# Optimization experiments

Hardware: AMD Instinct MI355X
Metric: run time of the kernel (lower is better)

The kernel has to match this reference:

```python
import jax, jax.numpy as jnp
import numpy as np
import math

B, S, D, H = 4, 2048, 1024, 16
DH = D // H  # 64
DFF = 4 * D
EPS = 1e-5


def layer_norm(x, g, b):
    mu = jnp.mean(x, axis=-1, keepdims=True)
    var = jnp.mean(jnp.square(x - mu), axis=-1, keepdims=True)
    return (x - mu) * jax.lax.rsqrt(var + EPS) * g + b


def apply_rope(xq, xk, freqs_cis):
    # xq, xk: [B, S, H, DH]; freqs_cis: [S, DH//2, 2] (cos, sin)
    cos = freqs_cis[None, :, None, :, 0]  # [1, S, 1, DH//2]
    sin = freqs_cis[None, :, None, :, 1]

    def rot(t):
        tr = t.reshape(*t.shape[:-1], DH // 2, 2)
        t0, t1 = tr[..., 0], tr[..., 1]
        o0 = t0 * cos - t1 * sin
        o1 = t0 * sin + t1 * cos
        return jnp.stack([o0, o1], axis=-1).reshape(t.shape)

    return rot(xq), rot(xk)


def setup_inputs() -> dict:
    key = jax.random.key(0)
    ks = jax.random.split(key, 12)
    x = jax.random.normal(ks[0], (B, S, D), dtype=jnp.float32)
    # rotary frequencies (theta = 10000), stored as (cos, sin)
    inv = 1.0 / (10000.0 ** (np.arange(0, DH, 2, dtype=np.float32) / DH))
    t = np.arange(S, dtype=np.float32)
    ang = np.outer(t, inv)  # [S, DH//2]
    freqs_cis = jnp.asarray(np.stack([np.cos(ang), np.sin(ang)], axis=-1))
    s = 1.0 / math.sqrt(D)
    sf = 1.0 / math.sqrt(DFF)
    return {
        "x": x,
        "freqs_cis": freqs_cis,
        "wq": jax.random.normal(ks[1], (D, D), dtype=jnp.float32) * s,
        "wk": jax.random.normal(ks[2], (D, D), dtype=jnp.float32) * s,
        "wv": jax.random.normal(ks[3], (D, D), dtype=jnp.float32) * s,
        "w_proj": jax.random.normal(ks[4], (D, D), dtype=jnp.float32) * s,
        "b_proj": jnp.zeros((D,), dtype=jnp.float32),
        "w_ff1": jax.random.normal(ks[5], (D, DFF), dtype=jnp.float32) * s,
        "b_ff1": jnp.zeros((DFF,), dtype=jnp.float32),
        "w_ff2": jax.random.normal(ks[6], (DFF, D), dtype=jnp.float32) * sf,
        "b_ff2": jnp.zeros((D,), dtype=jnp.float32),
        "ln1_g": jnp.ones((D,), dtype=jnp.float32),
        "ln1_b": jnp.zeros((D,), dtype=jnp.float32),
        "ln2_g": jnp.ones((D,), dtype=jnp.float32),
        "ln2_b": jnp.zeros((D,), dtype=jnp.float32),
    }


def reference(x, freqs_cis, wq, wk, wv, w_proj, b_proj, w_ff1, b_ff1, w_ff2,
              b_ff2, ln1_g, ln1_b, ln2_g, ln2_b):
    # --- attention block (pre-norm) ---
    h = layer_norm(x, ln1_g, ln1_b)
    xq = (h @ wq).reshape(B, S, H, DH)
    xk = (h @ wk).reshape(B, S, H, DH)
    xv = (h @ wv).reshape(B, S, H, DH)
    xq, xk = apply_rope(xq, xk, freqs_cis)
    # [B, H, S, S]
    att = jnp.einsum("bqhd,bkhd->bhqk", xq, xk) / math.sqrt(DH)
    att = jax.nn.softmax(att, axis=-1)
    out = jnp.einsum("bhqk,bkhd->bqhd", att, xv).reshape(B, S, D)
    x = x + out @ w_proj + b_proj
    # --- feed-forward block (pre-norm, GELU) ---
    h2 = layer_norm(x, ln2_g, ln2_b)
    ff = jax.nn.gelu(h2 @ w_ff1 + b_ff1, approximate=False) @ w_ff2 + b_ff2
    return x + ff
```

## Files before the change

### kernel.cpp

```cpp
#include <hip/hip_runtime.h>
#include <hip/hip_bf16.h>


#define Bb_ 4
#define Ss_ 2048
#define Dd_ 1024
#define Hh_ 16
#define DFF_ 4096

typedef __bf16 bf16x8 __attribute__((ext_vector_type(8)));
typedef float f32x4 __attribute__((ext_vector_type(4)));

static __device__ __forceinline__ unsigned short f2bf(float f) {
  union { float f; unsigned u; } v; v.f = f;
  unsigned r = v.u + 0x7FFF + ((v.u >> 16) & 1);
  return (unsigned short)(r >> 16);
}
static __device__ __forceinline__ float bf2f(unsigned short h) {
  union { unsigned u; float f; } v; v.u = ((unsigned)h) << 16;
  return v.f;
}
static __device__ __forceinline__ unsigned cvt_pk_bf16(float lo, float hi) {
  unsigned r;
  asm("v_cvt_pk_bf16_f32 %0, %1, %2" : "=v"(r) : "v"(lo), "v"(hi));
  return r;
}

static __device__ __forceinline__ void gl16(const unsigned short* g, void* l) {
  __builtin_amdgcn_global_load_lds(
      (const __attribute__((address_space(1))) void*)g,
      (__attribute__((address_space(3))) void*)l, 16, 0, 0);
}

__global__ __launch_bounds__(256) void ln_kernel(
    const float* __restrict__ x, const float* __restrict__ g,
    const float* __restrict__ bb, unsigned short* __restrict__ out)
{
  const int row = blockIdx.x;
  const int t = threadIdx.x;
  const float4 v = reinterpret_cast<const float4*>(x + (size_t)row * Dd_)[t];
  float s = v.x + v.y + v.z + v.w;
  float ss = v.x*v.x + v.y*v.y + v.z*v.z + v.w*v.w;
  #pragma unroll
  for (int o = 32; o; o >>= 1) { s += __shfl_down(s, o); ss += __shfl_down(ss, o); }
  __shared__ float red[8];
  if ((t & 63) == 0) { red[t >> 6] = s; red[4 + (t >> 6)] = ss; }
  __syncthreads();
  s = red[0] + red[1] + red[2] + red[3];
  ss = red[4] + red[5] + red[6] + red[7];
  const float mean = s * (1.f / Dd_);
  const float var = ss * (1.f / Dd_) - mean * mean;
  const float inv = rsqrtf(var + 1e-5f);
  const float4 gv = reinterpret_cast<const float4*>(g)[t];
  const float4 bv = reinterpret_cast<const float4*>(bb)[t];
  ushort4 o4;
  o4.x = f2bf((v.x - mean) * inv * gv.x + bv.x);
  o4.y = f2bf((v.y - mean) * inv * gv.y + bv.y);
  o4.z = f2bf((v.z - mean) * inv * gv.z + bv.z);
  o4.w = f2bf((v.w - mean) * inv * gv.w + bv.w);
  reinterpret_cast<ushort4*>(out + (size_t)row * Dd_)[t] = o4;
}

__global__ __launch_bounds__(256) void tconv_kernel(
    const float* __restrict__ src, unsigned short* __restrict__ dst, int K, int N)
{
  __shared__ float tile[32][33];
  const int bx = blockIdx.x, by = blockIdx.y;
  const int tx = threadIdx.x & 31, ty = threadIdx.x >> 5;
  #pragma unroll
  for (int i = 0; i < 4; i++)
    tile[ty + i * 8][tx] = src[(size_t)(by * 32 + ty + i * 8) * N + bx * 32 + tx];
  __syncthreads();
  #pragma unroll
  for (int i = 0; i < 4; i++)
    dst[(size_t)(bx * 32 + ty + i * 8) * K + by * 32 + tx] = f2bf(tile[tx][ty + i * 8]);
}

__global__ __launch_bounds__(256) void rope_kernel(
    unsigned short* __restrict__ qkv, const float* __restrict__ fc)
{
  const int c = blockIdx.x * 256 + threadIdx.x;
  const int row = c >> 8;
  const int rem = c & 255;
  const int qk = rem >> 7;
  const int e8 = rem & 127;
  const int s = row & (Ss_ - 1);
  const float4 f0 = *reinterpret_cast<const float4*>(fc + s * 64 + (e8 & 7) * 8);
  const float4 f1 = *reinterpret_cast<const float4*>(fc + s * 64 + (e8 & 7) * 8 + 4);
  unsigned short* p = qkv + (size_t)row * 3072 + qk * 1024 + e8 * 8;
  uint4 dv = *reinterpret_cast<const uint4*>(p);
  unsigned u[4] = {dv.x, dv.y, dv.z, dv.w};
  const float cs[8] = {f0.x, f0.y, f0.z, f0.w, f1.x, f1.y, f1.z, f1.w};
  #pragma unroll
  for (int j = 0; j < 4; j++) {
    const float t0 = bf2f((unsigned short)(u[j] & 0xffff));
    const float t1 = bf2f((unsigned short)(u[j] >> 16));
    const float cj = cs[2 * j], sj = cs[2 * j + 1];
    const float o0 = t0 * cj - t1 * sj;
    const float o1 = t0 * sj + t1 * cj;
    u[j] = (unsigned)f2bf(o0) | ((unsigned)f2bf(o1) << 16);
  }
  uint4 ov; ov.x = u[0]; ov.y = u[1]; ov.z = u[2]; ov.w = u[3];
  *reinterpret_cast<uint4*>(p) = ov;
}

__global__ __launch_bounds__(256) void vtrans_kernel(
    const unsigned short* __restrict__ qkv, unsigned short* __restrict__ vt)
{
  __shared__ unsigned short tile[64 * 64];
  const int st = blockIdx.x, h = blockIdx.y, b = blockIdx.z;
  const int t = threadIdx.x;
  const unsigned short* src = qkv + (size_t)(b * Ss_ + st * 64) * 3072 + 2048 + h * 64;
  {
    const int s = t >> 2;
    const int v = (s >> 3) & 7;
    #pragma unroll
    for (int j = 0; j < 2; j++) {
      const int col8 = (t & 3) * 2 + j;
      const uint4 d = *reinterpret_cast<const uint4*>(src + (size_t)s * 3072 + col8 * 8);
      *reinterpret_cast<uint4*>(&tile[s * 64 + ((col8 * 8) ^ (v * 8))]) = d;
    }
  }
  __syncthreads();
  unsigned short* dst = vt + (size_t)((b * 16 + h) * 64) * Ss_ + st * 64;
  #pragma unroll
  for (int it = 0; it < 2; it++) {
    const int c = t + it * 256;
    const int d = c >> 3, s8 = c & 7;
    unsigned short o[8];
    #pragma unroll
    for (int j = 0; j < 8; j++) {
      const int s = s8 * 8 + j;
      o[j] = tile[s * 64 + (d ^ (((s >> 3) & 7) * 8))];
    }
    *reinterpret_cast<uint4*>(dst + (size_t)d * Ss_ + s8 * 8) = *reinterpret_cast<uint4*>(o);
  }
}

template<int MODE>
__global__ __launch_bounds__(256) void gemm_kernel(
    const unsigned short* __restrict__ A,
    const unsigned short* __restrict__ BT,
    int K, int nbn, int N,
    const float* __restrict__ bias,
    const float* __restrict__ resid,
    void* __restrict__ out)
{
  __shared__ unsigned short As[2][128 * 64];
  __shared__ unsigned short Bs[2][128 * 64];
  const int t = threadIdx.x;

  const int nwg = gridDim.x;
  const int id = blockIdx.x;
  const int sid = (id & 7) * (nwg >> 3) + (id >> 3);
  const int bm = sid / nbn, bn = sid % nbn;

  const int w = t >> 6, lane = t & 63;
  const int lq = lane >> 4, lr = lane & 15;
  const int wm = (w >> 1) * 64, wn = (w & 1) * 64;
  const int srow = t >> 3, sg8 = t & 7;
  const int sw8 = sg8 ^ (srow & 7);

  const unsigned short* ag = A  + (size_t)(bm * 128 + srow) * K + sw8 * 8;
  const unsigned short* bg = BT + (size_t)(bn * 128 + srow) * K + sw8 * 8;

  char* AsB = (char*)As;
  char* BsB = (char*)Bs;
  const int csw = (lr & 7) * 8;
  int aoffB[2], boffB[2];
  aoffB[0] = (wm + lr) * 128 + 2 * ((lq * 8) ^ csw);
  aoffB[1] = (wm + lr) * 128 + 2 * ((32 + lq * 8) ^ csw);
  boffB[0] = (wn + lr) * 128 + 2 * ((lq * 8) ^ csw);
  boffB[1] = (wn + lr) * 128 + 2 * ((32 + lq * 8) ^ csw);
  const int sdstB = (srow * 64 + sg8 * 8) * 2;

  f32x4 acc[4][4] = {};
  const int nt = K >> 6;

#define STAGE7(BUF)                                                          \
  {                                                                          \
    _Pragma("unroll")                                                        \
    for (int i_ = 0; i_ < 4; i_++) {                                         \
      gl16(ag + (size_t)i_ * 32 * K, AsB + (BUF) * 16384 + sdstB + i_ * 4096); \
      gl16(bg + (size_t)i_ * 32 * K, BsB + (BUF) * 16384 + sdstB + i_ * 4096); \
    }                                                                        \
    ag += 64; bg += 64;                                                      \
  }

#define COMPUTE7(BUF)                                                        \
  {                                                                          \
    __builtin_amdgcn_s_setprio(1);                                           \
    _Pragma("unroll")                                                        \
    for (int kc_ = 0; kc_ < 2; kc_++) {                                      \
      bf16x8 af[4], bfr[4];                                                  \
      _Pragma("unroll")                                                      \
      for (int i_ = 0; i_ < 4; i_++) {                                       \
        af[i_]  = *reinterpret_cast<const bf16x8*>(AsB + (BUF) * 16384 + aoffB[kc_] + i_ * 2048); \
        bfr[i_] = *reinterpret_cast<const bf16x8*>(BsB + (BUF) * 16384 + boffB[kc_] + i_ * 2048); \
      }                                                                      \
      _Pragma("unroll")                                                      \
      for (int i_ = 0; i_ < 4; i_++)                                         \
        _Pragma("unroll")                                                    \
        for (int j_ = 0; j_ < 4; j_++)                                       \
          acc[i_][j_] = __builtin_amdgcn_mfma_f32_16x16x32_bf16(af[i_], bfr[j_], acc[i_][j_], 0, 0, 0); \
    }                                                                        \
    __builtin_amdgcn_s_setprio(0);                                           \
  }

  STAGE7(0);
  __syncthreads();
  for (int t0 = 0; t0 < nt; t0 += 2) {
    STAGE7(1);
    COMPUTE7(0);
    __syncthreads();
    if (t0 + 2 < nt) STAGE7(0);
    COMPUTE7(1);
    __syncthreads();
  }
#undef STAGE7
#undef COMPUTE7

  const int growbase = bm * 128 + wm + lq * 4;
  const int gcolbase = bn * 128 + wn + lr;
  #pragma unroll
  for (int j = 0; j < 4; j++) {
    const int col = gcolbase + j * 16;
    const float bj = (MODE != 0) ? bias[col] : 0.f;
    #pragma unroll
    for (int i = 0; i < 4; i++) {
      #pragma unroll
      for (int r = 0; r < 4; r++) {
        const int grow = growbase + i * 16 + r;
        const float v = acc[i][j][r];
        if (MODE == 0) {
          ((unsigned short*)out)[(size_t)grow * N + col] = f2bf(v);
        } else if (MODE == 1 || MODE == 3) {
          ((float*)out)[(size_t)grow * N + col] = v + bj + resid[(size_t)grow * N + col];
        } else {
          const float u = v + bj;
          const float gel = 0.5f * u * (1.f + erff(u * 0.70710678118654752f));
          ((unsigned short*)out)[(size_t)grow * N + col] = f2bf(gel);
        }
      }
    }
  }
}

__global__ __launch_bounds__(256) void attn_kernel(
    const unsigned short* __restrict__ qkv,
    const unsigned short* __restrict__ vt,
    unsigned short* __restrict__ attout)
{
  __shared__ unsigned short Ks[2][64 * 64];
  __shared__ unsigned short Vs[2][64 * 64];
  __shared__ unsigned short Ps[128 * 64];
  const int qt = blockIdx.x, h = blockIdx.y, b = blockIdx.z;
  const int t = threadIdx.x, w = t >> 6, lane = t & 63;
  const int lq = lane >> 4, lr = lane & 15;
  const int srow = t >> 3, sg8 = t & 7;

  const unsigned short* kg = qkv + (size_t)(b * Ss_) * 3072 + 1024 + h * 64;
  const unsigned short* vg = vt + (size_t)((b * 16 + h) * 64) * Ss_;

  bf16x8 aq[2][2];
  {
    const unsigned short* qg = qkv + (size_t)(b * Ss_ + qt * 128) * 3072 + h * 64;
    #pragma unroll
    for (int mt = 0; mt < 2; mt++)
      #pragma unroll
      for (int kc = 0; kc < 2; kc++)
        aq[mt][kc] = *reinterpret_cast<const bf16x8*>(
            qg + (size_t)(w * 32 + mt * 16 + lr) * 3072 + kc * 32 + lq * 8);
  }

  bf16x8 ones;
  #pragma unroll
  for (int j = 0; j < 8; j++) ones[j] = (__bf16)1.0f;

  f32x4 oacc[2][4] = {};
  f32x4 ssum[2] = {};

  const int g8s0 = sg8 ^ ((srow)      & 7);
  const int g8s1 = sg8 ^ ((srow + 32) & 7);

  {
    gl16(kg + (size_t)(srow)      * 3072 + g8s0 * 8, &Ks[0][(srow)      * 64 + sg8 * 8]);
    gl16(kg + (size_t)(srow + 32) * 3072 + g8s1 * 8, &Ks[0][(srow + 32) * 64 + sg8 * 8]);
    gl16(vg + (size_t)(srow)      * Ss_  + g8s0 * 8, &Vs[0][(srow)      * 64 + sg8 * 8]);
    gl16(vg + (size_t)(srow + 32) * Ss_  + g8s1 * 8, &Vs[0][(srow + 32) * 64 + sg8 * 8]);
  }
  __syncthreads();

  const float SC2 = 0.125f * 1.44269504088896f;

  for (int kt = 0; kt < Ss_ / 64; ++kt) {
    const int cur = kt & 1;
    if (kt < Ss_ / 64 - 1) {
      const int nb = cur ^ 1;
      const size_t ko = (size_t)((kt + 1) * 64);
      gl16(kg + (ko + srow)      * 3072 + g8s0 * 8, &Ks[nb][(srow)      * 64 + sg8 * 8]);
      gl16(kg + (ko + srow + 32) * 3072 + g8s1 * 8, &Ks[nb][(srow + 32) * 64 + sg8 * 8]);
      gl16(vg + (size_t)(srow)      * Ss_ + (kt + 1) * 64 + g8s0 * 8, &Vs[nb][(srow)      * 64 + sg8 * 8]);
      gl16(vg + (size_t)(srow + 32) * Ss_ + (kt + 1) * 64 + g8s1 * 8, &Vs[nb][(srow + 32) * 64 + sg8 * 8]);
    }

    f32x4 sacc[2][4] = {};
    #pragma unroll
    for (int kc = 0; kc < 2; kc++) {
      const int cofs = kc * 32 + lq * 8;
      const int swz = (lr & 7) * 8;
      bf16x8 kb[4];
      #pragma unroll
      for (int nf = 0; nf < 4; nf++)
        kb[nf] = *reinterpret_cast<const bf16x8*>(&Ks[cur][(nf * 16 + lr) * 64 + (cofs ^ swz)]);
      #pragma unroll
      for (int mt = 0; mt < 2; mt++)
        #pragma unroll
        for (int nf = 0; nf < 4; nf++)
          sacc[mt][nf] = __builtin_amdgcn_mfma_f32_16x16x32_bf16(kb[nf], aq[mt][kc], sacc[mt][nf], 0, 0, 0);
    }

    #pragma unroll
    for (int mt = 0; mt < 2; mt++) {
      const int qrow = w * 32 + mt * 16 + lr;
      char* prow = reinterpret_cast<char*>(Ps) + qrow * 128;
      const int sw = (lr & 7) << 4;
      #pragma unroll
      for (int nf = 0; nf < 4; nf++) {
        const float p0 = __builtin_amdgcn_exp2f(sacc[mt][nf][0] * SC2);
        const float p1 = __builtin_amdgcn_exp2f(sacc[mt][nf][1] * SC2);
        const float p2 = __builtin_amdgcn_exp2f(sacc[mt][nf][2] * SC2);
        const float p3 = __builtin_amdgcn_exp2f(sacc[mt][nf][3] * SC2);
        uint2 pw;
        pw.x = cvt_pk_bf16(p0, p1);
        pw.y = cvt_pk_bf16(p2, p3);
        *reinterpret_cast<uint2*>(prow + ((nf * 32 + lq * 8) ^ sw)) = pw;
      }
    }

    #pragma unroll
    for (int kc = 0; kc < 2; kc++) {
      const int cofs = kc * 32 + lq * 8;
      const int swz = (lr & 7) * 8;
      bf16x8 pa[2], vb[4];
      #pragma unroll
      for (int mt = 0; mt < 2; mt++) {
        const int qrow = w * 32 + mt * 16 + lr;
        pa[mt] = *reinterpret_cast<const bf16x8*>(
            reinterpret_cast<const char*>(Ps) + qrow * 128 + ((kc * 64 + lq * 16) ^ ((lr & 7) << 4)));
      }
      #pragma unroll
      for (int mt = 0; mt < 2; mt++)
        ssum[mt] = __builtin_amdgcn_mfma_f32_16x16x32_bf16(pa[mt], ones, ssum[mt], 0, 0, 0);
      #pragma unroll
      for (int nf = 0; nf < 4; nf++)
        vb[nf] = *reinterpret_cast<const bf16x8*>(&Vs[cur][(nf * 16 + lr) * 64 + (cofs ^ swz)]);
      #pragma unroll
      for (int mt = 0; mt < 2; mt++)
        #pragma unroll
        for (int nf = 0; nf < 4; nf++)
          oacc[mt][nf] = __builtin_amdgcn_mfma_f32_16x16x32_bf16(pa[mt], vb[nf], oacc[mt][nf], 0, 0, 0);
    }

    __syncthreads();
  }

  #pragma unroll
  for (int mt = 0; mt < 2; mt++) {
    #pragma unroll
    for (int r = 0; r < 4; r++) {
      const float inv = 1.f / ssum[mt][r];
      const int grow = b * Ss_ + qt * 128 + w * 32 + mt * 16 + lq * 4 + r;
      #pragma unroll
      for (int nf = 0; nf < 4; nf++)
        attout[(size_t)grow * Dd_ + h * 64 + nf * 16 + lr] = f2bf(oacc[mt][nf][r] * inv);
    }
  }
}

extern "C" void kernel_launch(void* const* d_in, const int* in_sizes, int n_in,
                              void* d_out, int out_size, void* d_ws, size_t ws_size,
                              hipStream_t stream) {
  const float* x      = (const float*)d_in[0];
  const float* fc     = (const float*)d_in[1];
  const float* wq     = (const float*)d_in[2];
  const float* wk     = (const float*)d_in[3];
  const float* wv     = (const float*)d_in[4];
  const float* w_proj = (const float*)d_in[5];
  const float* b_proj = (const float*)d_in[6];
  const float* w_ff1  = (const float*)d_in[7];
  const float* b_ff1  = (const float*)d_in[8];
  const float* w_ff2  = (const float*)d_in[9];
  const float* b_ff2  = (const float*)d_in[10];
  const float* ln1_g  = (const float*)d_in[11];
  const float* ln1_b  = (const float*)d_in[12];
  const float* ln2_g  = (const float*)d_in[13];
  const float* ln2_b  = (const float*)d_in[14];

  char* ws = (char*)d_ws;
  unsigned short* hb     = (unsigned short*)(ws);
  unsigned short* wqkvT  = (unsigned short*)(ws + 16777216ull);
  unsigned short* wprojT = (unsigned short*)(ws + 23068672ull);
  unsigned short* wff1T  = (unsigned short*)(ws + 25165824ull);
  unsigned short* wff2T  = (unsigned short*)(ws + 33554432ull);
  float*          x2     = (float*)(ws + 41943040ull);
  unsigned short* vtb    = (unsigned short*)(ws + 41943040ull);
  unsigned short* attoutb= (unsigned short*)(ws + 75497472ull);
  unsigned short* qkvb   = (unsigned short*)(ws + 92274688ull);
  unsigned short* ff1b   = qkvb;

  dim3 blk(256);

  tconv_kernel<<<dim3(32, 32), blk, 0, stream>>>(wq, wqkvT, 1024, 1024);
  tconv_kernel<<<dim3(32, 32), blk, 0, stream>>>(wk, wqkvT + 1024 * 1024, 1024, 1024);
  tconv_kernel<<<dim3(32, 32), blk, 0, stream>>>(wv, wqkvT + 2 * 1024 * 1024, 1024, 1024);
  tconv_kernel<<<dim3(32, 32), blk, 0, stream>>>(w_proj, wprojT, 1024, 1024);
  tconv_kernel<<<dim3(128, 32), blk, 0, stream>>>(w_ff1, wff1T, 1024, 4096);
  tconv_kernel<<<dim3(32, 128), blk, 0, stream>>>(w_ff2, wff2T, 4096, 1024);

  ln_kernel<<<8192, blk, 0, stream>>>(x, ln1_g, ln1_b, hb);
  gemm_kernel<0><<<1536, blk, 0, stream>>>(hb, wqkvT, 1024, 24, 3072, nullptr, nullptr, qkvb);
  rope_kernel<<<8192, blk, 0, stream>>>(qkvb, fc);
  vtrans_kernel<<<dim3(32, 16, 4), blk, 0, stream>>>(qkvb, vtb);
  attn_kernel<<<dim3(16, 16, 4), blk, 0, stream>>>(qkvb, vtb, attoutb);
  gemm_kernel<1><<<512, blk, 0, stream>>>(attoutb, wprojT, 1024, 8, 1024, b_proj, x, x2);
  ln_kernel<<<8192, blk, 0, stream>>>(x2, ln2_g, ln2_b, hb);
  gemm_kernel<2><<<2048, blk, 0, stream>>>(hb, wff1T, 1024, 32, 4096, b_ff1, nullptr, ff1b);
  gemm_kernel<3><<<512, blk, 0, stream>>>(ff1b, wff2T, 4096, 8, 1024, b_ff2, x2, (float*)d_out);
}
```

Before: 428.3 us.

## Add 256x256-tile 8-wave GEMM for QKV and FF1 projections

Adds a new GEMM kernel with 256x256 output tiles, 512 threads and 64 KB LDS double buffering. It uses explicit barrier/waitcnt interleaving so the global-to-LDS loads of the next K tile overlap MFMA work, and raises MFMA priority with setprio. The QKV and FF1 GEMMs now use it, which halves operand traffic per flop compared with the 128x128 kernel. The cost is lower occupancy (one block per CU, high register use). With only 384 and 512 blocks the grid may not balance well across CUs.

```diff
diff --git a/kernel.cpp b/kernel.cpp
--- a/kernel.cpp
+++ b/kernel.cpp
@@ -134,6 +134,150 @@
       o[j] = tile[s * 64 + (d ^ (((s >> 3) & 7) * 8))];
     }
     *reinterpret_cast<uint4*>(dst + (size_t)d * Ss_ + s8 * 8) = *reinterpret_cast<uint4*>(o);
+  }
+}
+
+template<int MODE>
+__global__ __launch_bounds__(512, 1) void gemm256_kernel(
+    const unsigned short* __restrict__ A,
+    const unsigned short* __restrict__ BT,
+    int K, int nbn, int N,
+    const float* __restrict__ bias,
+    void* __restrict__ out)
+{
+  __shared__ __align__(16) unsigned short As[2][256 * 64];
+  __shared__ __align__(16) unsigned short Bs[2][256 * 64];
+  const int t = threadIdx.x;
+
+  const int nwg = gridDim.x;
+  const int id = blockIdx.x;
+  const int sid = (id & 7) * (nwg >> 3) + (id >> 3);
+  const int bm = sid / nbn, bn = sid % nbn;
+
+  const int w = t >> 6, lane = t & 63;
+  const int lq = lane >> 4, lr = lane & 15;
+  const int wr = w >> 2, wc = w & 3;
+  const int srow = t >> 3, sg8 = t & 7;
+  const int sw8 = sg8 ^ (srow & 7);
+
+  const unsigned short* ag = A  + (size_t)(bm * 256 + srow) * K + sw8 * 8;
+  const unsigned short* bg = BT + (size_t)(bn * 256 + srow) * K + sw8 * 8;
+
+  char* AsB = (char*)As;
+  char* BsB = (char*)Bs;
+  const int aRow = (wr * 128 + lr) * 128;
+  const int bRow = (wc * 64 + lr) * 128;
+  int cofs[2];
+  cofs[0] = 2 * ((lq * 8) ^ ((lr & 7) * 8));
+  cofs[1] = 2 * (((32 + lq * 8)) ^ ((lr & 7) * 8));
+  const int sdst = (srow * 64 + sg8 * 8) * 2;
+
+  f32x4 acc[8][4] = {};
+  bf16x8 a0, a1, a2, a3, b0, b1, b2, b3;
+  const int nt = K >> 6;
+
+#define BAR_   __builtin_amdgcn_s_barrier()
+#define LGKM0_ { asm volatile("s_waitcnt lgkmcnt(0)" ::: "memory"); __builtin_amdgcn_sched_barrier(0); }
+#define VM0_   { asm volatile("s_waitcnt vmcnt(0)" ::: "memory"); __builtin_amdgcn_sched_barrier(0); }
+
+#define RD_A(D, MH, KC)                                                       \
+  a0 = *reinterpret_cast<const bf16x8*>(AsB + (D) * 32768 + aRow + (MH) * 8192 + 0 * 2048 + cofs[KC]); \
+  a1 = *reinterpret_cast<const bf16x8*>(AsB + (D) * 32768 + aRow + (MH) * 8192 + 1 * 2048 + cofs[KC]); \
+  a2 = *reinterpret_cast<const bf16x8*>(AsB + (D) * 32768 + aRow + (MH) * 8192 + 2 * 2048 + cofs[KC]); \
+  a3 = *reinterpret_cast<const bf16x8*>(AsB + (D) * 32768 + aRow + (MH) * 8192 + 3 * 2048 + cofs[KC]);
+
+#define RD_B(D, KC)                                                           \
+  b0 = *reinterpret_cast<const bf16x8*>(BsB + (D) * 32768 + bRow + 0 * 2048 + cofs[KC]); \
+  b1 = *reinterpret_cast<const bf16x8*>(BsB + (D) * 32768 + bRow + 1 * 2048 + cofs[KC]); \
+  b2 = *reinterpret_cast<const bf16x8*>(BsB + (D) * 32768 + bRow + 2 * 2048 + cofs[KC]); \
+  b3 = *reinterpret_cast<const bf16x8*>(BsB + (D) * 32768 + bRow + 3 * 2048 + cofs[KC]);
+
+#define MM_(MH)                                                               \
+  {                                                                           \
+    __builtin_amdgcn_s_setprio(1);                                            \
+    acc[(MH)*4+0][0] = __builtin_amdgcn_mfma_f32_16x16x32_bf16(a0, b0, acc[(MH)*4+0][0], 0, 0, 0); \
+    acc[(MH)*4+0][1] = __builtin_amdgcn_mfma_f32_16x16x32_bf16(a0, b1, acc[(MH)*4+0][1], 0, 0, 0); \
+    acc[(MH)*4+0][2] = __builtin_amdgcn_mfma_f32_16x16x32_bf16(a0, b2, acc[(MH)*4+0][2], 0, 0, 0); \
+    acc[(MH)*4+0][3] = __builtin_amdgcn_mfma_f32_16x16x32_bf16(a0, b3, acc[(MH)*4+0][3], 0, 0, 0); \
+    acc[(MH)*4+1][0] = __builtin_amdgcn_mfma_f32_16x16x32_bf16(a1, b0, acc[(MH)*4+1][0], 0, 0, 0); \
+    acc[(MH)*4+1][1] = __builtin_amdgcn_mfma_f32_16x16x32_bf16(a1, b1, acc[(MH)*4+1][1], 0, 0, 0); \
+    acc[(MH)*4+1][2] = __builtin_amdgcn_mfma_f32_16x16x32_bf16(a1, b2, acc[(MH)*4+1][2], 0, 0, 0); \
+    acc[(MH)*4+1][3] = __builtin_amdgcn_mfma_f32_16x16x32_bf16(a1, b3, acc[(MH)*4+1][3], 0, 0, 0); \
+    acc[(MH)*4+2][0] = __builtin_amdgcn_mfma_f32_16x16x32_bf16(a2, b0, acc[(MH)*4+2][0], 0, 0, 0); \
+    acc[(MH)*4+2][1] = __builtin_amdgcn_mfma_f32_16x16x32_bf16(a2, b1, acc[(MH)*4+2][1], 0, 0, 0); \
+    acc[(MH)*4+2][2] = __builtin_amdgcn_mfma_f32_16x16x32_bf16(a2, b2, acc[(MH)*4+2][2], 0, 0, 0); \
+    acc[(MH)*4+2][3] = __builtin_amdgcn_mfma_f32_16x16x32_bf16(a2, b3, acc[(MH)*4+2][3], 0, 0, 0); \
+    acc[(MH)*4+3][0] = __builtin_amdgcn_mfma_f32_16x16x32_bf16(a3, b0, acc[(MH)*4+3][0], 0, 0, 0); \
+    acc[(MH)*4+3][1] = __builtin_amdgcn_mfma_f32_16x16x32_bf16(a3, b1, acc[(MH)*4+3][1], 0, 0, 0); \
+    acc[(MH)*4+3][2] = __builtin_amdgcn_mfma_f32_16x16x32_bf16(a3, b2, acc[(MH)*4+3][2], 0, 0, 0); \
+    acc[(MH)*4+3][3] = __builtin_amdgcn_mfma_f32_16x16x32_bf16(a3, b3, acc[(MH)*4+3][3], 0, 0, 0); \
+    __builtin_amdgcn_s_setprio(0);                                            \
+  }
+
+#define STG_A(D)                                                              \
+  gl16(ag,                   AsB + (D) * 32768 + sdst);                       \
+  gl16(ag + (size_t) 64 * K, AsB + (D) * 32768 + sdst + 8192);                \
+  gl16(ag + (size_t)128 * K, AsB + (D) * 32768 + sdst + 16384);               \
+  gl16(ag + (size_t)192 * K, AsB + (D) * 32768 + sdst + 24576);
+
+#define STG_B(D)                                                              \
+  gl16(bg,                   BsB + (D) * 32768 + sdst);                       \
+  gl16(bg + (size_t) 64 * K, BsB + (D) * 32768 + sdst + 8192);                \
+  gl16(bg + (size_t)128 * K, BsB + (D) * 32768 + sdst + 16384);               \
+  gl16(bg + (size_t)192 * K, BsB + (D) * 32768 + sdst + 24576);
+
+#define KSTEP(D, HN)                                                          \
+  {                                                                           \
+     RD_A(D, 0, 0); RD_B(D, 0); if (HN) { STG_A((D) ^ 1); }           \
+    BAR_; LGKM0_; MM_(0); BAR_;                                               \
+     RD_A(D, 1, 0);             if (HN) { STG_B((D) ^ 1); }           \
+    BAR_; LGKM0_; MM_(1); BAR_;                                               \
+     RD_A(D, 0, 1); RD_B(D, 1);                                       \
+    BAR_; LGKM0_; MM_(0); BAR_;                                               \
+     RD_A(D, 1, 1);                                                   \
+    BAR_; LGKM0_; MM_(1); VM0_; BAR_;                                         \
+    ag += 64; bg += 64;                                                       \
+  }
+
+  STG_A(0); STG_B(0);
+  ag += 64; bg += 64;
+  VM0_; BAR_;
+
+  for (int t0 = 0; t0 < nt - 2; t0 += 2) { KSTEP(0, 1); KSTEP(1, 1); }
+  KSTEP(0, 1);
+  KSTEP(1, 0);
+
+#undef KSTEP
+#undef STG_A
+#undef STG_B
+#undef MM_
+#undef RD_A
+#undef RD_B
+#undef BAR_
+#undef LGKM0_
+#undef VM0_
+
+  const int growbase = bm * 256 + wr * 128 + lq * 4;
+  const int gcolbase = bn * 256 + wc * 64 + lr;
+  #pragma unroll
+  for (int j = 0; j < 4; j++) {
+    const int col = gcolbase + j * 16;
+    const float bj = (MODE != 0) ? bias[col] : 0.f;
+    #pragma unroll
+    for (int i = 0; i < 8; i++) {
+      #pragma unroll
+      for (int r = 0; r < 4; r++) {
+        const int grow = growbase + i * 16 + r;
+        const float v = acc[i][j][r];
+        if (MODE == 0) {
+          ((unsigned short*)out)[(size_t)grow * N + col] = f2bf(v);
+        } else {
+          const float u = v + bj;
+          const float gel = 0.5f * u * (1.f + erff(u * 0.70710678118654752f));
+          ((unsigned short*)out)[(size_t)grow * N + col] = f2bf(gel);
+        }
+      }
+    }
   }
 }
 
@@ -225,22 +369,14 @@
   #pragma unroll
   for (int j = 0; j < 4; j++) {
     const int col = gcolbase + j * 16;
-    const float bj = (MODE != 0) ? bias[col] : 0.f;
+    const float bj = bias[col];
     #pragma unroll
     for (int i = 0; i < 4; i++) {
       #pragma unroll
       for (int r = 0; r < 4; r++) {
         const int grow = growbase + i * 16 + r;
-        const float v = acc[i][j][r];
-        if (MODE == 0) {
-          ((unsigned short*)out)[(size_t)grow * N + col] = f2bf(v);
-        } else if (MODE == 1 || MODE == 3) {
-          ((float*)out)[(size_t)grow * N + col] = v + bj + resid[(size_t)grow * N + col];
-        } else {
-          const float u = v + bj;
-          const float gel = 0.5f * u * (1.f + erff(u * 0.70710678118654752f));
-          ((unsigned short*)out)[(size_t)grow * N + col] = f2bf(gel);
-        }
+        ((float*)out)[(size_t)grow * N + col] =
+            acc[i][j][r] + bj + resid[(size_t)grow * N + col];
       }
     }
   }
@@ -410,6 +546,7 @@
   unsigned short* ff1b   = qkvb;
 
   dim3 blk(256);
+  dim3 blk512(512);
 
   tconv_kernel<<<dim3(32, 32), blk, 0, stream>>>(wq, wqkvT, 1024, 1024);
   tconv_kernel<<<dim3(32, 32), blk, 0, stream>>>(wk, wqkvT + 1024 * 1024, 1024, 1024);
@@ -419,12 +556,12 @@
   tconv_kernel<<<dim3(32, 128), blk, 0, stream>>>(w_ff2, wff2T, 4096, 1024);
 
   ln_kernel<<<8192, blk, 0, stream>>>(x, ln1_g, ln1_b, hb);
-  gemm_kernel<0><<<1536, blk, 0, stream>>>(hb, wqkvT, 1024, 24, 3072, nullptr, nullptr, qkvb);
+  gemm256_kernel<0><<<384, blk512, 0, stream>>>(hb, wqkvT, 1024, 12, 3072, nullptr, qkvb);
   rope_kernel<<<8192, blk, 0, stream>>>(qkvb, fc);
   vtrans_kernel<<<dim3(32, 16, 4), blk, 0, stream>>>(qkvb, vtb);
   attn_kernel<<<dim3(16, 16, 4), blk, 0, stream>>>(qkvb, vtb, attoutb);
   gemm_kernel<1><<<512, blk, 0, stream>>>(attoutb, wprojT, 1024, 8, 1024, b_proj, x, x2);
   ln_kernel<<<8192, blk, 0, stream>>>(x2, ln2_g, ln2_b, hb);
-  gemm_kernel<2><<<2048, blk, 0, stream>>>(hb, wff1T, 1024, 32, 4096, b_ff1, nullptr, ff1b);
+  gemm256_kernel<2><<<512, blk512, 0, stream>>>(hb, wff1T, 1024, 16, 4096, b_ff1, ff1b);
   gemm_kernel<3><<<512, blk, 0, stream>>>(ff1b, wff2T, 4096, 8, 1024, b_ff2, x2, (float*)d_out);
 }
```

Result: slower. 450.2 us (+5.1%).

## Fuse RoPE and V transpose into QKV GEMM epilogue

Applied to the files above, without the earlier changes.

Removes the separate rope and V-transpose kernels. The QKV GEMM epilogue now applies rotary embedding to the Q/K columns, pairing adjacent columns with a lane shuffle, and writes V directly in transposed layout to the vt buffer. This saves two extra passes over the QKV activations and two launches. In exchange the epilogue does per-element frequency loads and scattered 8-byte transposed stores.

```diff
diff --git a/kernel.cpp b/kernel.cpp
--- a/kernel.cpp
+++ b/kernel.cpp
@@ -76,67 +76,6 @@
     dst[(size_t)(bx * 32 + ty + i * 8) * K + by * 32 + tx] = f2bf(tile[tx][ty + i * 8]);
 }
 
-__global__ __launch_bounds__(256) void rope_kernel(
-    unsigned short* __restrict__ qkv, const float* __restrict__ fc)
-{
-  const int c = blockIdx.x * 256 + threadIdx.x;
-  const int row = c >> 8;
-  const int rem = c & 255;
-  const int qk = rem >> 7;
-  const int e8 = rem & 127;
-  const int s = row & (Ss_ - 1);
-  const float4 f0 = *reinterpret_cast<const float4*>(fc + s * 64 + (e8 & 7) * 8);
-  const float4 f1 = *reinterpret_cast<const float4*>(fc + s * 64 + (e8 & 7) * 8 + 4);
-  unsigned short* p = qkv + (size_t)row * 3072 + qk * 1024 + e8 * 8;
-  uint4 dv = *reinterpret_cast<const uint4*>(p);
-  unsigned u[4] = {dv.x, dv.y, dv.z, dv.w};
-  const float cs[8] = {f0.x, f0.y, f0.z, f0.w, f1.x, f1.y, f1.z, f1.w};
-  #pragma unroll
-  for (int j = 0; j < 4; j++) {
-    const float t0 = bf2f((unsigned short)(u[j] & 0xffff));
-    const float t1 = bf2f((unsigned short)(u[j] >> 16));
-    const float cj = cs[2 * j], sj = cs[2 * j + 1];
-    const float o0 = t0 * cj - t1 * sj;
-    const float o1 = t0 * sj + t1 * cj;
-    u[j] = (unsigned)f2bf(o0) | ((unsigned)f2bf(o1) << 16);
-  }
-  uint4 ov; ov.x = u[0]; ov.y = u[1]; ov.z = u[2]; ov.w = u[3];
-  *reinterpret_cast<uint4*>(p) = ov;
-}
-
-__global__ __launch_bounds__(256) void vtrans_kernel(
-    const unsigned short* __restrict__ qkv, unsigned short* __restrict__ vt)
-{
-  __shared__ unsigned short tile[64 * 64];
-  const int st = blockIdx.x, h = blockIdx.y, b = blockIdx.z;
-  const int t = threadIdx.x;
-  const unsigned short* src = qkv + (size_t)(b * Ss_ + st * 64) * 3072 + 2048 + h * 64;
-  {
-    const int s = t >> 2;
-    const int v = (s >> 3) & 7;
-    #pragma unroll
-    for (int j = 0; j < 2; j++) {
-      const int col8 = (t & 3) * 2 + j;
-      const uint4 d = *reinterpret_cast<const uint4*>(src + (size_t)s * 3072 + col8 * 8);
-      *reinterpret_cast<uint4*>(&tile[s * 64 + ((col8 * 8) ^ (v * 8))]) = d;
-    }
-  }
-  __syncthreads();
-  unsigned short* dst = vt + (size_t)((b * 16 + h) * 64) * Ss_ + st * 64;
-  #pragma unroll
-  for (int it = 0; it < 2; it++) {
-    const int c = t + it * 256;
-    const int d = c >> 3, s8 = c & 7;
-    unsigned short o[8];
-    #pragma unroll
-    for (int j = 0; j < 8; j++) {
-      const int s = s8 * 8 + j;
-      o[j] = tile[s * 64 + (d ^ (((s >> 3) & 7) * 8))];
-    }
-    *reinterpret_cast<uint4*>(dst + (size_t)d * Ss_ + s8 * 8) = *reinterpret_cast<uint4*>(o);
-  }
-}
-
 template<int MODE>
 __global__ __launch_bounds__(256) void gemm_kernel(
     const unsigned short* __restrict__ A,
@@ -144,7 +83,9 @@
     int K, int nbn, int N,
     const float* __restrict__ bias,
     const float* __restrict__ resid,
-    void* __restrict__ out)
+    void* __restrict__ out,
+    const float* __restrict__ fcp,
+    void* __restrict__ out2)
 {
   __shared__ unsigned short As[2][128 * 64];
   __shared__ unsigned short Bs[2][128 * 64];
@@ -222,24 +163,66 @@
 
   const int growbase = bm * 128 + wm + lq * 4;
   const int gcolbase = bn * 128 + wn + lr;
-  #pragma unroll
-  for (int j = 0; j < 4; j++) {
-    const int col = gcolbase + j * 16;
-    const float bj = (MODE != 0) ? bias[col] : 0.f;
-    #pragma unroll
-    for (int i = 0; i < 4; i++) {
-      #pragma unroll
-      for (int r = 0; r < 4; r++) {
-        const int grow = growbase + i * 16 + r;
-        const float v = acc[i][j][r];
-        if (MODE == 0) {
-          ((unsigned short*)out)[(size_t)grow * N + col] = f2bf(v);
-        } else if (MODE == 1 || MODE == 3) {
-          ((float*)out)[(size_t)grow * N + col] = v + bj + resid[(size_t)grow * N + col];
-        } else {
-          const float u = v + bj;
-          const float gel = 0.5f * u * (1.f + erff(u * 0.70710678118654752f));
-          ((unsigned short*)out)[(size_t)grow * N + col] = f2bf(gel);
+
+  if (MODE == 0) {
+    if (bn < 16) {
+      const float sgn = (lr & 1) ? 1.f : -1.f;
+      #pragma unroll
+      for (int j = 0; j < 4; j++) {
+        const int col = gcolbase + j * 16;
+        const int ip = (col & 63) & ~1;
+        #pragma unroll
+        for (int i = 0; i < 4; i++) {
+          #pragma unroll
+          for (int r = 0; r < 4; r++) {
+            const int grow = growbase + i * 16 + r;
+            const int s = grow & (Ss_ - 1);
+            const float2 cs = *reinterpret_cast<const float2*>(fcp + (size_t)s * 64 + ip);
+            const float v = acc[i][j][r];
+            const float p = __shfl_xor(v, 1);
+            const float o = v * cs.x + sgn * p * cs.y;
+            ((unsigned short*)out)[(size_t)grow * N + col] = f2bf(o);
+          }
+        }
+      }
+    } else {
+      #pragma unroll
+      for (int j = 0; j < 4; j++) {
+        const int vcol = gcolbase + j * 16 - 2048;
+        const int h = vcol >> 6, d = vcol & 63;
+        #pragma unroll
+        for (int i = 0; i < 4; i++) {
+          const int g0 = growbase + i * 16;
+          const int b = g0 >> 11, s0 = g0 & (Ss_ - 1);
+          ushort4 o4;
+          o4.x = f2bf(acc[i][j][0]);
+          o4.y = f2bf(acc[i][j][1]);
+          o4.z = f2bf(acc[i][j][2]);
+          o4.w = f2bf(acc[i][j][3]);
+          unsigned short* vr = (unsigned short*)out2 +
+              ((size_t)((b * 16 + h) * 64 + d)) * Ss_ + s0;
+          *reinterpret_cast<ushort4*>(vr) = o4;
+        }
+      }
+    }
+  } else {
+    #pragma unroll
+    for (int j = 0; j < 4; j++) {
+      const int col = gcolbase + j * 16;
+      const float bj = bias[col];
+      #pragma unroll
+      for (int i = 0; i < 4; i++) {
+        #pragma unroll
+        for (int r = 0; r < 4; r++) {
+          const int grow = growbase + i * 16 + r;
+          const float v = acc[i][j][r];
+          if (MODE == 1 || MODE == 3) {
+            ((float*)out)[(size_t)grow * N + col] = v + bj + resid[(size_t)grow * N + col];
+          } else {
+            const float u = v + bj;
+            const float gel = 0.5f * u * (1.f + erff(u * 0.70710678118654752f));
+            ((unsigned short*)out)[(size_t)grow * N + col] = f2bf(gel);
+          }
         }
       }
     }
@@ -419,12 +402,10 @@
   tconv_kernel<<<dim3(32, 128), blk, 0, stream>>>(w_ff2, wff2T, 4096, 1024);
 
   ln_kernel<<<8192, blk, 0, stream>>>(x, ln1_g, ln1_b, hb);
-  gemm_kernel<0><<<1536, blk, 0, stream>>>(hb, wqkvT, 1024, 24, 3072, nullptr, nullptr, qkvb);
-  rope_kernel<<<8192, blk, 0, stream>>>(qkvb, fc);
-  vtrans_kernel<<<dim3(32, 16, 4), blk, 0, stream>>>(qkvb, vtb);
+  gemm_kernel<0><<<1536, blk, 0, stream>>>(hb, wqkvT, 1024, 24, 3072, nullptr, nullptr, qkvb, fc, vtb);
   attn_kernel<<<dim3(16, 16, 4), blk, 0, stream>>>(qkvb, vtb, attoutb);
-  gemm_kernel<1><<<512, blk, 0, stream>>>(attoutb, wprojT, 1024, 8, 1024, b_proj, x, x2);
+  gemm_kernel<1><<<512, blk, 0, stream>>>(attoutb, wprojT, 1024, 8, 1024, b_proj, x, x2, nullptr, nullptr);
   ln_kernel<<<8192, blk, 0, stream>>>(x2, ln2_g, ln2_b, hb);
-  gemm_kernel<2><<<2048, blk, 0, stream>>>(hb, wff1T, 1024, 32, 4096, b_ff1, nullptr, ff1b);
-  gemm_kernel<3><<<512, blk, 0, stream>>>(ff1b, wff2T, 4096, 8, 1024, b_ff2, x2, (float*)d_out);
-}
+  gemm_kernel<2><<<2048, blk, 0, stream>>>(hb, wff1T, 1024, 32, 4096, b_ff1, nullptr, ff1b, nullptr, nullptr);
+  gemm_kernel<3><<<512, blk, 0, stream>>>(ff1b, wff2T, 4096, 8, 1024, b_ff2, x2, (float*)d_out, nullptr, nullptr);
+}
```

Result: no change. 421.1 us (-1.7%).
